# Performance work log

Measured on AMD Instinct MI355X. Metric: run time of the kernel, lower is better.

## Reference

```python
import jax, jax.numpy as jnp
import numpy as np

ACTION_SCALE = 0.01
LOG_STD_MIN, LOG_STD_MAX = -20.0, 2.0


def setup_inputs() -> dict:
    key = jax.random.key(0)
    k1, k2, k3 = jax.random.split(key, 3)
    B, N, D = 8, 1024, 128
    kv = jax.random.normal(k1, (B, N, 4 * D), dtype=jnp.float32)
    positions = jax.random.normal(k2, (B, N, 3), dtype=jnp.float32)
    eps = jax.random.normal(k3, (B, N, 3), dtype=jnp.float32)  # standard-normal sample for rsample
    return {"kv": kv, "positions": positions, "eps": eps}


def reference(kv, positions, eps):
    # Split Atomwise output into mean/std key-value embeddings: each [B, N, D]
    k_mu, v_mu, k_sigma, v_sigma = jnp.split(kv, 4, axis=-1)

    # Low-rank attention-like pairwise scores: [B, N, N]
    rel_shifts_mean = jnp.einsum("bid,bjd->bij", k_mu, v_mu)
    rel_shifts_log_std = jnp.einsum("bid,bjd->bij", k_sigma, v_sigma)

    # All-pairs unit displacement vectors: [B, N, N, 3]
    P = positions[:, :, None, :] - positions[:, None, :, :]
    norm = jnp.linalg.norm(P, axis=-1) + 1e-8
    P = P / norm[..., None]

    # Weighted sum over the j axis (torch dim=-2): [B, N, 3]
    actions_mean = jnp.einsum("bijc,bij->bic", P, rel_shifts_mean)
    actions_log_std = jnp.clip(
        jnp.einsum("bijc,bij->bic", P, rel_shifts_log_std), LOG_STD_MIN, LOG_STD_MAX
    )
    actions_std = jnp.exp(actions_log_std)

    # TanhNormal rsample (training branch) with externally supplied noise eps
    pre_tanh = actions_mean + actions_std * eps
    actions = jnp.tanh(pre_tanh)

    # Normal log-prob minus tanh log-det-Jacobian
    normal_lp = (
        -0.5 * ((pre_tanh - actions_mean) / actions_std) ** 2
        - actions_log_std
        - 0.5 * jnp.log(2.0 * jnp.pi)
    )
    log_det = (
        2.0 * jnp.log(2.0)
        + jax.nn.log_sigmoid(2.0 * pre_tanh)
        + jax.nn.log_sigmoid(-2.0 * pre_tanh)
    )
    log_prob = jnp.sum(normal_lp - log_det, axis=(1, 2))[:, None]  # [B, 1]

    actions = actions * ACTION_SCALE
    # change-of-variables correction for the action_scale factor
    n_dims = pre_tanh.shape[1] * pre_tanh.shape[2]
    log_prob = log_prob - n_dims * jnp.log(ACTION_SCALE)
    return actions, log_prob
```

## Files before the change

### kernel.cpp

```cpp
#include <hip/hip_runtime.h>
#include <math.h>


#define NTOK 1024
#define LPCONST 14147.0828114f

typedef __bf16 bf16x8 __attribute__((ext_vector_type(8)));
typedef float f32x4 __attribute__((ext_vector_type(4)));
#define MFMA(a, b, c) __builtin_amdgcn_mfma_f32_16x16x32_bf16(a, b, c, 0, 0, 0)

__device__ __forceinline__ unsigned short to_bf16(float x) {
    return (unsigned short)((__float_as_uint(x) + 0x8000u) >> 16);
}

__device__ __forceinline__ float softplusf(float z) {
    return z > 20.f ? z : log1pf(expf(z));
}

__global__ __launch_bounds__(256) void prepass_kernel(
    const float* __restrict__ kv, unsigned short* __restrict__ frag,
    float* __restrict__ out)
{
    const int t = blockIdx.x * 256 + threadIdx.x;
    if (t < 8) out[8 * NTOK * 3 + t] = LPCONST;

    const int lane = t & 63;
    const int kc   = (t >> 6) & 3;
    const int tile = (t >> 8) & 63;
    const int b    = (t >> 14) & 7;
    const int side = t >> 17;

    const int row = tile * 16 + (lane & 15);
    const int kof = kc * 32 + (lane >> 4) * 8;
    const float* gp = kv + ((size_t)b * NTOK + row) * 512 + side * 128 + kof;
    const float4 m0 = *(const float4*)gp;
    const float4 m1 = *(const float4*)(gp + 4);
    const float4 s0 = *(const float4*)(gp + 256);
    const float4 s1 = *(const float4*)(gp + 260);

    unsigned short* cp = frag + (size_t)side * 2097152 +
                         (size_t)(b * 64 + tile) * 4096 + kc * 1024 + lane * 8;
    ushort4 h0, h1;
    h0.x = to_bf16(m0.x); h0.y = to_bf16(m0.y); h0.z = to_bf16(m0.z); h0.w = to_bf16(m0.w);
    h1.x = to_bf16(m1.x); h1.y = to_bf16(m1.y); h1.z = to_bf16(m1.z); h1.w = to_bf16(m1.w);
    *(ushort4*)(cp + 0) = h0; *(ushort4*)(cp + 4) = h1;
    h0.x = to_bf16(s0.x); h0.y = to_bf16(s0.y); h0.z = to_bf16(s0.z); h0.w = to_bf16(s0.w);
    h1.x = to_bf16(s1.x); h1.y = to_bf16(s1.y); h1.z = to_bf16(s1.z); h1.w = to_bf16(s1.w);
    *(ushort4*)(cp + 512) = h0; *(ushort4*)(cp + 516) = h1;
}

__global__ __launch_bounds__(512) void actor_kernel(
    const unsigned short* __restrict__ frag, const float* __restrict__ pos,
    float* __restrict__ partial)
{
    const int t = threadIdx.x;
    const int w = t >> 6;
    const int lane = t & 63;
    const int q = lane >> 4;
    const int r16 = lane & 15;
    const int b   = blockIdx.x & 7;
    const int jh  = (blockIdx.x >> 3) & 3;
    const int ibx = blockIdx.x >> 5;
    const int i0 = ibx * 64;

    const unsigned short* fragK = frag;
    const unsigned short* fragV = frag + 2097152;
    const float* posb = pos + (size_t)b * NTOK * 3;

    __shared__ unsigned short sK[16384];
    __shared__ float spos[NTOK * 3];
    __shared__ float wacc[8 * 64 * 6];

    {
        const unsigned short* kg =
            fragK + (size_t)(b * 64 + ibx * 4) * 4096 + t * 32;
        #pragma unroll
        for (int r = 0; r < 4; ++r)
            *(ushort4*)&sK[t * 32 + r * 4] = *(const ushort4*)(kg + r * 4);
        const unsigned short* kg2 = kg + 16;
        #pragma unroll
        for (int r = 0; r < 4; ++r)
            *(ushort4*)&sK[t * 32 + 16 + r * 4] = *(const ushort4*)(kg2 + r * 4);
    }
    for (int u = t; u < 768; u += 512)
        *(float4*)&spos[u * 4] = *(const float4*)&posb[u * 4];
    __syncthreads();

    float pix[4], piy[4], piz[4];
    #pragma unroll
    for (int tile = 0; tile < 4; ++tile) {
        pix[tile] = spos[(i0 + tile * 16 + r16) * 3 + 0];
        piy[tile] = spos[(i0 + tile * 16 + r16) * 3 + 1];
        piz[tile] = spos[(i0 + tile * 16 + r16) * 3 + 2];
    }

    float am[4][3] = {};
    float al[4][3] = {};

    const int jtile0 = jh * 16 + w * 2;
    const unsigned short* vbase =
        fragV + (size_t)(b * 64 + jtile0) * 4096 + lane * 8;
    const int klofs = lane * 8;

    #pragma unroll
    for (int jt = 0; jt < 2; ++jt) {
        const unsigned short* vp = vbase + jt * 4096;
        f32x4 accm[4], accs[4];
        #pragma unroll
        for (int tile = 0; tile < 4; ++tile) {
            accm[tile] = (f32x4){0.f, 0.f, 0.f, 0.f};
            accs[tile] = (f32x4){0.f, 0.f, 0.f, 0.f};
        }
        #pragma unroll
        for (int kc = 0; kc < 4; ++kc) {
            const bf16x8 Vm = *(const bf16x8*)(vp + kc * 1024);
            const bf16x8 Vs = *(const bf16x8*)(vp + kc * 1024 + 512);
            #pragma unroll
            for (int tile = 0; tile < 4; ++tile) {
                const bf16x8 Km = *(const bf16x8*)&sK[tile * 4096 + kc * 1024 + klofs];
                const bf16x8 Ks = *(const bf16x8*)&sK[tile * 4096 + kc * 1024 + 512 + klofs];
                accm[tile] = MFMA(Vm, Km, accm[tile]);
                accs[tile] = MFMA(Vs, Ks, accs[tile]);
            }
        }
        const int jbase = (jtile0 + jt) * 16 + q * 4;
        #pragma unroll
        for (int reg = 0; reg < 4; ++reg) {
            const float* pj = &spos[(jbase + reg) * 3];
            const float pjx = pj[0], pjy = pj[1], pjz = pj[2];
            #pragma unroll
            for (int tile = 0; tile < 4; ++tile) {
                const float dx = pix[tile] - pjx;
                const float dy = piy[tile] - pjy;
                const float dz = piz[tile] - pjz;
                const float d2 = dx * dx + dy * dy + dz * dz;
                const float inv = d2 > 0.f ? rsqrtf(d2) : 0.f;
                const float wm = accm[tile][reg] * inv;
                const float ws = accs[tile][reg] * inv;
                am[tile][0] = fmaf(dx, wm, am[tile][0]);
                am[tile][1] = fmaf(dy, wm, am[tile][1]);
                am[tile][2] = fmaf(dz, wm, am[tile][2]);
                al[tile][0] = fmaf(dx, ws, al[tile][0]);
                al[tile][1] = fmaf(dy, ws, al[tile][1]);
                al[tile][2] = fmaf(dz, ws, al[tile][2]);
            }
        }
    }

    #pragma unroll
    for (int tile = 0; tile < 4; ++tile)
        #pragma unroll
        for (int c = 0; c < 3; ++c) {
            float vm = am[tile][c], vl = al[tile][c];
            vm += __shfl_xor(vm, 16, 64); vm += __shfl_xor(vm, 32, 64);
            vl += __shfl_xor(vl, 16, 64); vl += __shfl_xor(vl, 32, 64);
            am[tile][c] = vm; al[tile][c] = vl;
        }

    if (lane < 16) {
        #pragma unroll
        for (int tile = 0; tile < 4; ++tile) {
            float* p = wacc + (w * 64 + tile * 16 + r16) * 6;
            p[0] = am[tile][0]; p[1] = am[tile][1]; p[2] = am[tile][2];
            p[3] = al[tile][0]; p[4] = al[tile][1]; p[5] = al[tile][2];
        }
    }
    __syncthreads();
    if (t < 384) {
        float v = 0.f;
        #pragma unroll
        for (int ww = 0; ww < 8; ++ww) v += wacc[ww * 384 + t];
        const int row = t / 6, c = t - row * 6;
        partial[((size_t)((jh * 8 + b) * NTOK) + i0 + row) * 6 + c] = v;
    }
}

__global__ __launch_bounds__(64) void actor_tail_kernel(
    const float* __restrict__ partial, const float* __restrict__ eps,
    float* __restrict__ out)
{
    const int b = blockIdx.x >> 4;
    const int i = (blockIdx.x & 15) * 64 + threadIdx.x;
    const int gi = b * NTOK + i;

    float am[3] = {}, al[3] = {};
    #pragma unroll
    for (int jh = 0; jh < 4; ++jh) {
        const float* p = partial + (((size_t)jh * 8 + b) * NTOK + i) * 6;
        const float2 v0 = *(const float2*)(p);
        const float2 v1 = *(const float2*)(p + 2);
        const float2 v2 = *(const float2*)(p + 4);
        am[0] += v0.x; am[1] += v0.y; am[2] += v1.x;
        al[0] += v1.y; al[1] += v2.x; al[2] += v2.y;
    }

    float lp = 0.f;
    #pragma unroll
    for (int c = 0; c < 3; ++c) {
        const float als = fminf(fmaxf(al[c], -20.f), 2.f);
        const float sd = expf(als);
        const float e = eps[gi * 3 + c];
        const float pre = fmaf(sd, e, am[c]);
        out[gi * 3 + c] = tanhf(pre) * 0.01f;
        const float t2 = 2.f * pre;
        lp += -0.5f * e * e - als - 2.3052328944f + softplusf(t2) + softplusf(-t2);
    }

    #pragma unroll
    for (int m = 1; m < 64; m <<= 1) lp += __shfl_xor(lp, m, 64);
    if (threadIdx.x == 0) atomicAdd(out + NTOK * 8 * 3 + b, lp);
}

extern "C" void kernel_launch(void* const* d_in, const int* in_sizes, int n_in,
                              void* d_out, int out_size, void* d_ws, size_t ws_size,
                              hipStream_t stream) {
    const float* kv = (const float*)d_in[0];
    const float* pos = (const float*)d_in[1];
    const float* eps = (const float*)d_in[2];
    float* out = (float*)d_out;
    unsigned short* frag = (unsigned short*)d_ws;
    float* partial = (float*)((char*)d_ws + 8388608);

    prepass_kernel<<<dim3(1024), 256, 0, stream>>>(kv, frag, out);
    actor_kernel<<<dim3(512), 512, 0, stream>>>(frag, pos, partial);
    actor_tail_kernel<<<dim3(128), 64, 0, stream>>>(partial, eps, out);
}
```

Measured before the change: 87.08 us.

## Fuse bf16 conversion prepass into actor kernel and use fast tail math

Measured after the change: 93.62 us. 7.5% more time.

```diff
diff --git a/kernel.cpp b/kernel.cpp
--- a/kernel.cpp
+++ b/kernel.cpp
@@ -7,51 +7,27 @@
 
 typedef __bf16 bf16x8 __attribute__((ext_vector_type(8)));
 typedef float f32x4 __attribute__((ext_vector_type(4)));
+typedef unsigned short ushort8v __attribute__((ext_vector_type(8)));
 #define MFMA(a, b, c) __builtin_amdgcn_mfma_f32_16x16x32_bf16(a, b, c, 0, 0, 0)
 
 __device__ __forceinline__ unsigned short to_bf16(float x) {
     return (unsigned short)((__float_as_uint(x) + 0x8000u) >> 16);
 }
 
-__device__ __forceinline__ float softplusf(float z) {
-    return z > 20.f ? z : log1pf(expf(z));
-}
-
-__global__ __launch_bounds__(256) void prepass_kernel(
-    const float* __restrict__ kv, unsigned short* __restrict__ frag,
-    float* __restrict__ out)
-{
-    const int t = blockIdx.x * 256 + threadIdx.x;
-    if (t < 8) out[8 * NTOK * 3 + t] = LPCONST;
-
-    const int lane = t & 63;
-    const int kc   = (t >> 6) & 3;
-    const int tile = (t >> 8) & 63;
-    const int b    = (t >> 14) & 7;
-    const int side = t >> 17;
-
-    const int row = tile * 16 + (lane & 15);
-    const int kof = kc * 32 + (lane >> 4) * 8;
-    const float* gp = kv + ((size_t)b * NTOK + row) * 512 + side * 128 + kof;
-    const float4 m0 = *(const float4*)gp;
-    const float4 m1 = *(const float4*)(gp + 4);
-    const float4 s0 = *(const float4*)(gp + 256);
-    const float4 s1 = *(const float4*)(gp + 260);
-
-    unsigned short* cp = frag + (size_t)side * 2097152 +
-                         (size_t)(b * 64 + tile) * 4096 + kc * 1024 + lane * 8;
-    ushort4 h0, h1;
-    h0.x = to_bf16(m0.x); h0.y = to_bf16(m0.y); h0.z = to_bf16(m0.z); h0.w = to_bf16(m0.w);
-    h1.x = to_bf16(m1.x); h1.y = to_bf16(m1.y); h1.z = to_bf16(m1.z); h1.w = to_bf16(m1.w);
-    *(ushort4*)(cp + 0) = h0; *(ushort4*)(cp + 4) = h1;
-    h0.x = to_bf16(s0.x); h0.y = to_bf16(s0.y); h0.z = to_bf16(s0.z); h0.w = to_bf16(s0.w);
-    h1.x = to_bf16(s1.x); h1.y = to_bf16(s1.y); h1.z = to_bf16(s1.z); h1.w = to_bf16(s1.w);
-    *(ushort4*)(cp + 512) = h0; *(ushort4*)(cp + 516) = h1;
+__device__ __forceinline__ ushort8v pack8(float4 a, float4 b) {
+    ushort8v u;
+    u[0] = to_bf16(a.x); u[1] = to_bf16(a.y); u[2] = to_bf16(a.z); u[3] = to_bf16(a.w);
+    u[4] = to_bf16(b.x); u[5] = to_bf16(b.y); u[6] = to_bf16(b.z); u[7] = to_bf16(b.w);
+    return u;
+}
+
+__device__ __forceinline__ bf16x8 cvt8(float4 a, float4 b) {
+    return __builtin_bit_cast(bf16x8, pack8(a, b));
 }
 
 __global__ __launch_bounds__(512) void actor_kernel(
-    const unsigned short* __restrict__ frag, const float* __restrict__ pos,
-    float* __restrict__ partial)
+    const float* __restrict__ kv, const float* __restrict__ pos,
+    float* __restrict__ partial, float* __restrict__ out)
 {
     const int t = threadIdx.x;
     const int w = t >> 6;
@@ -63,24 +39,33 @@
     const int ibx = blockIdx.x >> 5;
     const int i0 = ibx * 64;
 
-    const unsigned short* fragK = frag;
-    const unsigned short* fragV = frag + 2097152;
+    if (blockIdx.x < 8 && t == 0) out[8 * NTOK * 3 + blockIdx.x] = LPCONST;
+
+    const float* kvb  = kv + (size_t)b * NTOK * 512;
     const float* posb = pos + (size_t)b * NTOK * 3;
 
-    __shared__ unsigned short sK[16384];
-    __shared__ float spos[NTOK * 3];
+    __shared__ __align__(16) unsigned short sK[16384];
+    __shared__ __align__(16) float spos[NTOK * 3];
     __shared__ float wacc[8 * 64 * 6];
 
     {
-        const unsigned short* kg =
-            fragK + (size_t)(b * 64 + ibx * 4) * 4096 + t * 32;
-        #pragma unroll
-        for (int r = 0; r < 4; ++r)
-            *(ushort4*)&sK[t * 32 + r * 4] = *(const ushort4*)(kg + r * 4);
-        const unsigned short* kg2 = kg + 16;
-        #pragma unroll
-        for (int r = 0; r < 4; ++r)
-            *(ushort4*)&sK[t * 32 + 16 + r * 4] = *(const ushort4*)(kg2 + r * 4);
+        const int ri = t >> 3;
+        const int cg = t & 7;
+        const float* gp = kvb + (size_t)(i0 + ri) * 512 + cg * 16;
+        const float4 m0 = *(const float4*)(gp);
+        const float4 m1 = *(const float4*)(gp + 4);
+        const float4 m2 = *(const float4*)(gp + 8);
+        const float4 m3 = *(const float4*)(gp + 12);
+        const float4 s0 = *(const float4*)(gp + 256);
+        const float4 s1 = *(const float4*)(gp + 260);
+        const float4 s2 = *(const float4*)(gp + 264);
+        const float4 s3 = *(const float4*)(gp + 268);
+        unsigned short* dp = sK + (ri >> 4) * 4096 + (cg >> 1) * 1024
+                           + ((cg & 1) * 32 + (ri & 15)) * 8;
+        *(ushort8v*)(dp)       = pack8(m0, m1);
+        *(ushort8v*)(dp + 128) = pack8(m2, m3);
+        *(ushort8v*)(dp + 512) = pack8(s0, s1);
+        *(ushort8v*)(dp + 640) = pack8(s2, s3);
     }
     for (int u = t; u < 768; u += 512)
         *(float4*)&spos[u * 4] = *(const float4*)&posb[u * 4];
@@ -98,13 +83,12 @@
     float al[4][3] = {};
 
     const int jtile0 = jh * 16 + w * 2;
-    const unsigned short* vbase =
-        fragV + (size_t)(b * 64 + jtile0) * 4096 + lane * 8;
+    const float* vrow = kvb + (size_t)(jtile0 * 16 + r16) * 512 + 128 + q * 8;
     const int klofs = lane * 8;
 
     #pragma unroll
     for (int jt = 0; jt < 2; ++jt) {
-        const unsigned short* vp = vbase + jt * 4096;
+        const float* vp = vrow + (size_t)jt * 16 * 512;
         f32x4 accm[4], accs[4];
         #pragma unroll
         for (int tile = 0; tile < 4; ++tile) {
@@ -113,8 +97,12 @@
         }
         #pragma unroll
         for (int kc = 0; kc < 4; ++kc) {
-            const bf16x8 Vm = *(const bf16x8*)(vp + kc * 1024);
-            const bf16x8 Vs = *(const bf16x8*)(vp + kc * 1024 + 512);
+            const float4 vm0 = *(const float4*)(vp + kc * 32);
+            const float4 vm1 = *(const float4*)(vp + kc * 32 + 4);
+            const bf16x8 Vm = cvt8(vm0, vm1);
+            const float4 vs0 = *(const float4*)(vp + kc * 32 + 256);
+            const float4 vs1 = *(const float4*)(vp + kc * 32 + 260);
+            const bf16x8 Vs = cvt8(vs0, vs1);
             #pragma unroll
             for (int tile = 0; tile < 4; ++tile) {
                 const bf16x8 Km = *(const bf16x8*)&sK[tile * 4096 + kc * 1024 + klofs];
@@ -198,12 +186,14 @@
     #pragma unroll
     for (int c = 0; c < 3; ++c) {
         const float als = fminf(fmaxf(al[c], -20.f), 2.f);
-        const float sd = expf(als);
+        const float sd = __expf(als);
         const float e = eps[gi * 3 + c];
         const float pre = fmaf(sd, e, am[c]);
-        out[gi * 3 + c] = tanhf(pre) * 0.01f;
-        const float t2 = 2.f * pre;
-        lp += -0.5f * e * e - als - 2.3052328944f + softplusf(t2) + softplusf(-t2);
+        const float a2 = 2.f * fabsf(pre);
+        const float E = __expf(-a2);
+        const float th = (1.f - E) / (1.f + E);
+        out[gi * 3 + c] = copysignf(th, pre) * 0.01f;
+        lp += fmaf(-0.5f * e, e, -als) - 2.3052328944f + a2 + 2.f * __logf(1.f + E);
     }
 
     #pragma unroll
@@ -218,10 +208,8 @@
     const float* pos = (const float*)d_in[1];
     const float* eps = (const float*)d_in[2];
     float* out = (float*)d_out;
-    unsigned short* frag = (unsigned short*)d_ws;
-    float* partial = (float*)((char*)d_ws + 8388608);
-
-    prepass_kernel<<<dim3(1024), 256, 0, stream>>>(kv, frag, out);
-    actor_kernel<<<dim3(512), 512, 0, stream>>>(frag, pos, partial);
+    float* partial = (float*)d_ws;
+
+    actor_kernel<<<dim3(512), 512, 0, stream>>>(kv, pos, partial, out);
     actor_tail_kernel<<<dim3(128), 64, 0, stream>>>(partial, eps, out);
 }
```
